# Optimization experiments

Measured on AMD Instinct MI355X. Metric: run time of the kernel, lower is better.

The kernel has to match this reference:

```python
import jax, jax.numpy as jnp
import numpy as np
import math

DIM = 1024
ATTN_DIM = 1024
B, S = 2, 4096

def setup_inputs() -> dict:
    key = jax.random.key(0)
    k1, k2, k3 = jax.random.split(key, 3)
    x = jax.random.normal(k1, (B, S, DIM), dtype=jnp.float32)
    # qkv Linear(dim, 3*attn_dim, bias=True): weight [3*attn_dim, dim], bias [3*attn_dim]
    W_qkv = jax.random.normal(k2, (3 * ATTN_DIM, DIM), dtype=jnp.float32) * (1.0 / math.sqrt(DIM))
    b_qkv = jax.random.normal(k3, (3 * ATTN_DIM,), dtype=jnp.float32) * 0.01
    return {"x": x, "W_qkv": W_qkv, "b_qkv": b_qkv}

def reference(x, W_qkv, b_qkv):
    b, s, d = x.shape
    qkv = jnp.einsum('bsd,ed->bse', x, W_qkv) + b_qkv  # [B,S,3*attn_dim]
    q, k, v = jnp.split(qkv, 3, axis=-1)
    score = jnp.einsum('bqd,bkd->bqk', q, k)  # [B,S,S]
    # causal mask applied BEFORE scaling (matches original: -inf survives the divide)
    causal = jnp.tril(jnp.ones((s, s), dtype=bool))
    score = jnp.where(causal, score, -jnp.inf)
    attn = jax.nn.softmax(score / math.sqrt(ATTN_DIM), axis=-1)
    y = jnp.einsum('bqk,bkd->bqd', attn, v)  # [B,S,attn_dim]
    return y
```

## Files before the change

### kernel.cpp

```cpp
#include <hip/hip_runtime.h>
#include <cstdint>
#include <cstddef>

typedef __bf16 bf16;
typedef bf16 bf16x4 __attribute__((ext_vector_type(4)));
typedef bf16 bf16x8 __attribute__((ext_vector_type(8)));
typedef float f32x4 __attribute__((ext_vector_type(4)));

#define SEQ 4096
#define DIMD 1024
#define TILE_K1024 131072L
#define TILE_K4096 524288L
#define PC_BATCH   8650752L

__device__ __forceinline__ int swz(int r, int c) {
    return r * 32 + (((((c >> 3) ^ (r >> 1)) & 3)) << 3) + (c & 7);
}

__device__ __forceinline__ void async16(void* lds, const void* g) {
    __builtin_amdgcn_global_load_lds(
        (__attribute__((address_space(1))) void*)g,
        (__attribute__((address_space(3))) void*)lds,
        16, 0, 0);
}

__device__ __forceinline__ void gemm_core(
    const bf16* __restrict__ At, const bf16* __restrict__ Bt,
    int k0, int k1, f32x4 acc[4][4])
{
    __shared__ bf16 lt[2][2][4096];
    const int tid  = threadIdx.x;
    const int lane = tid & 63;
    const int wid  = tid >> 6;
    const int wm   = (wid >> 1) * 64;
    const int wn   = (wid & 1) * 64;
    const int lr   = lane & 15;
    const int q    = lane >> 4;

    int offA[4], offB[4];
#pragma unroll
    for (int mi = 0; mi < 4; ++mi) {
        const int rA = wm + mi * 16 + lr;
        offA[mi] = rA * 32 + ((((rA >> 1) ^ q) & 3) << 3);
    }
#pragma unroll
    for (int ni = 0; ni < 4; ++ni) {
        const int rB = wn + ni * 16 + lr;
        offB[ni] = rB * 32 + ((((rB >> 1) ^ q) & 3) << 3);
    }

    const int t8 = tid * 8;

#define STAGE(kk, c) do { \
        const bf16* _sa = At + (long)(kk) * 4096; \
        const bf16* _sb = Bt + (long)(kk) * 4096; \
        async16(&lt[c][0][t8],        _sa + t8); \
        async16(&lt[c][0][2048 + t8], _sa + 2048 + t8); \
        async16(&lt[c][1][t8],        _sb + t8); \
        async16(&lt[c][1][2048 + t8], _sb + 2048 + t8); \
    } while (0)

    STAGE(k0, 0);
    if (k0 + 1 < k1) STAGE(k0 + 1, 1);

    for (int kk = k0; kk < k1; ++kk) {
        const int cur = (kk - k0) & 1;
        if (kk + 1 < k1) { asm volatile("s_waitcnt vmcnt(4)" ::: "memory"); }
        else             { asm volatile("s_waitcnt vmcnt(0)" ::: "memory"); }
        __builtin_amdgcn_s_barrier();
        __builtin_amdgcn_sched_barrier(0);

        bf16x8 af[4], bfr[4];
#pragma unroll
        for (int mi = 0; mi < 4; ++mi)
            af[mi] = *(const bf16x8*)&lt[cur][0][offA[mi]];
#pragma unroll
        for (int ni = 0; ni < 4; ++ni)
            bfr[ni] = *(const bf16x8*)&lt[cur][1][offB[ni]];

        __builtin_amdgcn_s_setprio(1);
#pragma unroll
        for (int mi = 0; mi < 4; ++mi)
#pragma unroll
            for (int ni = 0; ni < 4; ++ni)
                acc[mi][ni] = __builtin_amdgcn_mfma_f32_16x16x32_bf16(
                    af[mi], bfr[ni], acc[mi][ni], 0, 0, 0);
        __builtin_amdgcn_s_setprio(0);
        __builtin_amdgcn_sched_barrier(0);
        __builtin_amdgcn_s_barrier();
        if (kk + 2 < k1) STAGE(kk + 2, cur);
    }
#undef STAGE
}

__global__ __launch_bounds__(256) void cvt_all_kernel(
    const float* __restrict__ x, const float* __restrict__ W,
    bf16* __restrict__ xt, bf16* __restrict__ wt, float* __restrict__ sums)
{
    const int g = blockIdx.x, tid = threadIdx.x;
    if (g >= 11264) { sums[(g - 11264) * 256 + tid] = 0.0f; return; }
    const float* in; bf16* out; int i;
    if (g < 8192) { in = x; out = xt; i = g * 256 + tid; }
    else          { in = W; out = wt; i = (g - 8192) * 256 + tid; }
    const float4 v = ((const float4*)in)[i];
    const int j = i * 4, row = j >> 10, col = j & 1023;
    const long o = (long)(row >> 7) * TILE_K1024 + (col >> 5) * 4096
                 + swz(row & 127, col & 31);
    bf16x4 ov = { (bf16)v.x, (bf16)v.y, (bf16)v.z, (bf16)v.w };
    *(bf16x4*)&out[o] = ov;
}

__global__ __launch_bounds__(256) void qkv_gemm(
    const bf16* __restrict__ xt, const bf16* __restrict__ wt,
    const float* __restrict__ bias,
    bf16* __restrict__ Qt, bf16* __restrict__ Kt, bf16* __restrict__ Vtt)
{
    const int b = blockIdx.x, x = b & 7, r = b >> 3;
    const int mt = x * 8 + r / 24, wnid = r % 24;
    const int bm = mt * 128, bn = wnid * 128;

    f32x4 acc[4][4] = {};
    gemm_core(xt + (long)mt * TILE_K1024, wt + (long)wnid * TILE_K1024, 0, 32, acc);

    const int tid = threadIdx.x, lane = tid & 63, wid = tid >> 6;
    const int wm = (wid >> 1) * 64, wn = (wid & 1) * 64;
    const int lr = lane & 15, q4 = (lane >> 4) * 4;
#pragma unroll
    for (int ni = 0; ni < 4; ++ni) {
        const int n = bn + wn + ni * 16 + lr;
        const float bv = bias[n];
#pragma unroll
        for (int mi = 0; mi < 4; ++mi) {
            const int m0 = bm + wm + mi * 16 + q4;
            if (n < 2048) {
                bf16* dst = (n < 1024) ? Qt : Kt;
                const int c = n & 1023;
#pragma unroll
                for (int rr = 0; rr < 4; ++rr) {
                    const int m = m0 + rr;
                    dst[(long)(m >> 7) * TILE_K1024 + (c >> 5) * 4096
                        + swz(m & 127, c & 31)] = (bf16)(acc[mi][ni][rr] + bv);
                }
            } else {
                const int bb = m0 >> 12, s = m0 & 4095, d = n - 2048;
                bf16x4 o = { (bf16)(acc[mi][ni][0] + bv), (bf16)(acc[mi][ni][1] + bv),
                             (bf16)(acc[mi][ni][2] + bv), (bf16)(acc[mi][ni][3] + bv) };
                *(bf16x4*)&Vtt[(long)bb * 4194304 + (long)(d >> 7) * TILE_K4096
                               + (s >> 5) * 4096 + swz(d & 127, s & 31)] = o;
            }
        }
    }
}

__global__ __launch_bounds__(256) void score_kernel(
    const bf16* __restrict__ Qt, const bf16* __restrict__ Kt,
    bf16* __restrict__ Pc, float* __restrict__ sums)
{
    const int b = blockIdx.x, x = b & 7;
    int r = b >> 3;
    const int bz = r / 66, batch = bz;
    r %= 66;
    int qt, kt;
    const int s0 = x + 1;
    if (r < s0)           { qt = x;      kt = r; }
    else if (r < 33)      { qt = 31 - x; kt = r - s0; }
    else if (r < 42 + x)  { qt = x + 8;  kt = r - 33; }
    else                  { qt = 23 - x; kt = r - 42 - x; }

    bf16* Pb = Pc + (long)bz * PC_BATCH + (long)(qt * (qt + 1) / 2 + kt) * 16384;
    float* sb = sums + (long)batch * SEQ;

    f32x4 acc[4][4] = {};
    gemm_core(Qt + (long)(batch * 32 + qt) * TILE_K1024,
              Kt + (long)(batch * 32 + kt) * TILE_K1024, 0, 32, acc);

    const int tid = threadIdx.x, lane = tid & 63, wid = tid >> 6;
    const int wm = (wid >> 1) * 64, wn = (wid & 1) * 64;
    const int lr = lane & 15, q4 = (lane >> 4) * 4;
#pragma unroll
    for (int mi = 0; mi < 4; ++mi) {
#pragma unroll
        for (int rr = 0; rr < 4; ++rr) {
            const int ql = wm + mi * 16 + q4 + rr;
            const int q  = qt * 128 + ql;
            float rsum = 0.0f;
#pragma unroll
            for (int ni = 0; ni < 4; ++ni) {
                const int kl  = wn + ni * 16 + lr;
                const int key = kt * 128 + kl;
                const float s = acc[mi][ni][rr] * 0.03125f;
                const float p = (key <= q) ? __expf(s) : 0.0f;
                const bf16 pb = (bf16)p;
                Pb[(kl >> 5) * 4096 + swz(ql, kl & 31)] = pb;
                rsum += (float)pb;
            }
            rsum += __shfl_xor(rsum, 1);
            rsum += __shfl_xor(rsum, 2);
            rsum += __shfl_xor(rsum, 4);
            rsum += __shfl_xor(rsum, 8);
            if (lr == 0) atomicAdd(&sb[q], rsum);
        }
    }
}

__device__ const unsigned char pv_sched[96] = {
     15, 125,  28,  44,  25,  54,  86,  51,  83, 112,   4,   3,
     47,  93,  60,  12,  57,  22, 118,  19, 115,  80,  36,  35,
     31,  61,  92, 122,  89, 119,  10,  41,  18,  48,   5,   2,
     63,  29, 124,  90, 121,  87,  42,   9,  50,  16,  37,  34,
     95,  46,  13,  58,  24,  55,  21, 116,  82, 113,   7,   0,
    127,  14,  45,  26,  56,  23,  53,  84, 114,  81,  39,  32,
     30, 126,  27, 123,  88,  43,  85,  52,   8,  49,   6,   1,
     62,  94,  59,  91, 120,  11, 117,  20,  40,  17,  38,  33,
};

__global__ __launch_bounds__(256) void pv_kernel(
    const bf16* __restrict__ Pc, const bf16* __restrict__ Vtt,
    const float* __restrict__ sums, float* __restrict__ Y,
    float* __restrict__ part)
{
    const int b = blockIdx.x, x = b & 7, t = b >> 3;
    const int j = t >> 3, dt = t & 7;
    const int e = pv_sched[x * 12 + j];
    const int qt = e & 31, bz = (e >> 5) & 1, c = e >> 6;
    const int full = (qt + 1) * 4, half = (qt + 1) * 2;
    int k0, k1;
    if (qt < 16) { k0 = 0; k1 = full; }
    else { k0 = c ? half : 0; k1 = c ? full : half; }
    const int batch = bz;

    f32x4 acc[4][4] = {};
    gemm_core(Pc + (long)bz * PC_BATCH + (long)(qt * (qt + 1) / 2) * 16384,
              Vtt + (long)batch * 4194304 + (long)dt * TILE_K4096, k0, k1, acc);

    const int tid = threadIdx.x, lane = tid & 63, wid = tid >> 6;
    const int wm = (wid >> 1) * 64, wn = (wid & 1) * 64;
    const int lr = lane & 15, q4 = (lane >> 4) * 4;
#pragma unroll
    for (int mi = 0; mi < 4; ++mi) {
#pragma unroll
        for (int rr = 0; rr < 4; ++rr) {
            const int q = qt * 128 + wm + mi * 16 + q4 + rr;
            const float iv = 1.0f / sums[(long)batch * SEQ + q];
#pragma unroll
            for (int ni = 0; ni < 4; ++ni) {
                const int d = dt * 128 + wn + ni * 16 + lr;
                const float v = acc[mi][ni][rr] * iv;
                if (c == 0)
                    Y[(long)batch * 4194304 + (long)q * DIMD + d] = v;
                else
                    part[(long)bz * 2097152 + (long)(q - 2048) * DIMD + d] = v;
            }
        }
    }
}

__global__ __launch_bounds__(256) void combine_kernel(
    float* __restrict__ Y, const float* __restrict__ part)
{
    const long g = (long)blockIdx.x * 256 + threadIdx.x;
    const long e4 = g * 4;
    const int bz = (int)(e4 >> 21);
    const long rem = e4 & 2097151;
    float4 a = *(const float4*)&Y[(long)bz * 4194304 + 2097152 + rem];
    const float4 p = *(const float4*)&part[e4];
    a.x += p.x; a.y += p.y; a.z += p.z; a.w += p.w;
    *(float4*)&Y[(long)bz * 4194304 + 2097152 + rem] = a;
}

extern "C" void kernel_launch(void* const* d_in, const int* in_sizes, int n_in,
                              void* d_out, int out_size, void* d_ws, size_t ws_size,
                              hipStream_t stream)
{
    const float* x    = (const float*)d_in[0];
    const float* W    = (const float*)d_in[1];
    const float* bqkv = (const float*)d_in[2];
    float* out = (float*)d_out;
    char* ws = (char*)d_ws;

    bf16* Pc   = (bf16*)ws;
    bf16* xt   = (bf16*)ws;
    bf16* wt   = (bf16*)(ws + 16 * 1024 * 1024);
    bf16* Kt   = (bf16*)(ws + 34603008);
    bf16* Vtt  = (bf16*)(ws + 51380224);
    float* sums = (float*)(ws + 68157440);
    bf16* Qt   = (bf16*)d_out;
    float* part = (float*)Kt;

    cvt_all_kernel<<<11296, 256, 0, stream>>>(x, W, xt, wt, sums);
    qkv_gemm<<<1536, 256, 0, stream>>>(xt, wt, bqkv, Qt, Kt, Vtt);
    score_kernel<<<1056, 256, 0, stream>>>(Qt, Kt, Pc, sums);
    pv_kernel<<<768, 256, 0, stream>>>(Pc, Vtt, sums, out, part);
    combine_kernel<<<4096, 256, 0, stream>>>(out, part);
}
```

Baseline: 235.9 us.

## Enlarge QKV GEMM tile to 256x256 with 8 waves and triple-buffered async loads

The QKV projection GEMM moves from 128x128 tiles with 256 threads to 256x256 tiles with 512 threads. Each wave computes a 128x64 sub-tile with 8x4 MFMA accumulators. K-slices are staged through a three-deep LDS ring using global_load_lds and explicit vmcnt waits, and MFMA issue is given higher scheduling priority. This cuts global and L2 traffic per FLOP and overlaps loads with compute. The cost is higher register pressure, 96KB of LDS per block, and only 384 blocks, which may leave CUs underfilled.

Result: slower. 276.6 us (+17.3%).

```diff
diff --git a/kernel.cpp b/kernel.cpp
--- a/kernel.cpp
+++ b/kernel.cpp
@@ -110,28 +110,95 @@
     *(bf16x4*)&out[o] = ov;
 }
 
-__global__ __launch_bounds__(256) void qkv_gemm(
+__global__ __launch_bounds__(512, 2) void qkv_gemm(
     const bf16* __restrict__ xt, const bf16* __restrict__ wt,
     const float* __restrict__ bias,
     bf16* __restrict__ Qt, bf16* __restrict__ Kt, bf16* __restrict__ Vtt)
 {
+    __shared__ bf16 lt[3][4][4096];
+
     const int b = blockIdx.x, x = b & 7, r = b >> 3;
-    const int mt = x * 8 + r / 24, wnid = r % 24;
-    const int bm = mt * 128, bn = wnid * 128;
-
-    f32x4 acc[4][4] = {};
-    gemm_core(xt + (long)mt * TILE_K1024, wt + (long)wnid * TILE_K1024, 0, 32, acc);
-
-    const int tid = threadIdx.x, lane = tid & 63, wid = tid >> 6;
-    const int wm = (wid >> 1) * 64, wn = (wid & 1) * 64;
-    const int lr = lane & 15, q4 = (lane >> 4) * 4;
+    const int mt2 = x * 4 + r / 12, nt2 = r % 12;
+
+    const bf16* A0 = xt + (long)(2 * mt2) * TILE_K1024;
+    const bf16* A1 = A0 + TILE_K1024;
+    const bf16* B0 = wt + (long)(2 * nt2) * TILE_K1024;
+    const bf16* B1 = B0 + TILE_K1024;
+
+    const int tid  = threadIdx.x;
+    const int lane = tid & 63;
+    const int wid  = tid >> 6;
+    const int wr   = wid >> 2;
+    const int wc   = wid & 3;
+    const int lr   = lane & 15;
+    const int q    = lane >> 4;
+    const int t8   = tid * 8;
+
+    int offA[8], offB[4];
+#pragma unroll
+    for (int mi = 0; mi < 8; ++mi) {
+        const int rA = mi * 16 + lr;
+        offA[mi] = rA * 32 + ((((rA >> 1) ^ q) & 3) << 3);
+    }
 #pragma unroll
     for (int ni = 0; ni < 4; ++ni) {
-        const int n = bn + wn + ni * 16 + lr;
+        const int rB = (wc & 1) * 64 + ni * 16 + lr;
+        offB[ni] = rB * 32 + ((((rB >> 1) ^ q) & 3) << 3);
+    }
+    const int bslot = 2 + (wc >> 1);
+
+    f32x4 acc[8][4] = {};
+
+#define STG(kk, c) do { \
+        const long ko = (long)(kk) * 4096 + t8; \
+        async16(&lt[c][0][t8], A0 + ko); \
+        async16(&lt[c][1][t8], A1 + ko); \
+        async16(&lt[c][2][t8], B0 + ko); \
+        async16(&lt[c][3][t8], B1 + ko); \
+    } while (0)
+
+    STG(0, 0); STG(1, 1); STG(2, 2);
+
+    int cur = 0;
+    for (int kk = 0; kk < 32; ++kk) {
+        if      (kk + 2 < 32) { asm volatile("s_waitcnt vmcnt(8)" ::: "memory"); }
+        else if (kk + 1 < 32) { asm volatile("s_waitcnt vmcnt(4)" ::: "memory"); }
+        else                  { asm volatile("s_waitcnt vmcnt(0)" ::: "memory"); }
+        __builtin_amdgcn_s_barrier();
+        __builtin_amdgcn_sched_barrier(0);
+
+        bf16x8 af[8], bfr[4];
+#pragma unroll
+        for (int mi = 0; mi < 8; ++mi)
+            af[mi] = *(const bf16x8*)&lt[cur][wr][offA[mi]];
+#pragma unroll
+        for (int ni = 0; ni < 4; ++ni)
+            bfr[ni] = *(const bf16x8*)&lt[cur][bslot][offB[ni]];
+
+        __builtin_amdgcn_s_setprio(1);
+#pragma unroll
+        for (int mi = 0; mi < 8; ++mi)
+#pragma unroll
+            for (int ni = 0; ni < 4; ++ni)
+                acc[mi][ni] = __builtin_amdgcn_mfma_f32_16x16x32_bf16(
+                    af[mi], bfr[ni], acc[mi][ni], 0, 0, 0);
+        __builtin_amdgcn_s_setprio(0);
+        __builtin_amdgcn_sched_barrier(0);
+        __builtin_amdgcn_s_barrier();
+        if (kk + 3 < 32) STG(kk + 3, cur);
+        cur = (cur == 2) ? 0 : cur + 1;
+    }
+#undef STG
+
+    const int q4 = q * 4;
+    const int bm = mt2 * 256, bn = nt2 * 256;
+#pragma unroll
+    for (int ni = 0; ni < 4; ++ni) {
+        const int n = bn + wc * 64 + ni * 16 + lr;
         const float bv = bias[n];
 #pragma unroll
-        for (int mi = 0; mi < 4; ++mi) {
-            const int m0 = bm + wm + mi * 16 + q4;
+        for (int mi = 0; mi < 8; ++mi) {
+            const int m0 = bm + wr * 128 + mi * 16 + q4;
             if (n < 2048) {
                 bf16* dst = (n < 1024) ? Qt : Kt;
                 const int c = n & 1023;
@@ -288,7 +355,7 @@
     float* part = (float*)Kt;
 
     cvt_all_kernel<<<11296, 256, 0, stream>>>(x, W, xt, wt, sums);
-    qkv_gemm<<<1536, 256, 0, stream>>>(xt, wt, bqkv, Qt, Kt, Vtt);
+    qkv_gemm<<<384, 512, 0, stream>>>(xt, wt, bqkv, Qt, Kt, Vtt);
     score_kernel<<<1056, 256, 0, stream>>>(Qt, Kt, Pc, sums);
     pv_kernel<<<768, 256, 0, stream>>>(Pc, Vtt, sums, out, part);
     combine_kernel<<<4096, 256, 0, stream>>>(out, part);
```
